# Kernel optimization log

Hardware: AMD Instinct MI355X
Metric: run time of the kernel (lower is better)

Reference implementation:

```python
import jax, jax.numpy as jnp
import numpy as np

N = 50000
E = 800000
IN_CH = 128
HID = 64
HEADS = 4
NEG_SLOPE_GAT = 0.2   # PyG GATConv default negative_slope
NEG_SLOPE_ACT = 0.01  # nn.LeakyReLU default
LN_EPS = 1e-5


def segment_softmax(logits, seg, num):
    # softmax over edges grouped by destination node (PyG softmax semantics)
    m = jax.ops.segment_max(logits, seg, num_segments=num)
    m = jnp.where(jnp.isfinite(m), m, 0.0)
    e = jnp.exp(logits - m[seg])
    s = jax.ops.segment_sum(e, seg, num_segments=num)
    return e / (s[seg] + 1e-16)


def gat_conv(x, edge_index, W, a_src, a_dst, b, heads, out_ch):
    n = x.shape[0]
    loop = jnp.arange(n)
    src = jnp.concatenate([edge_index[0], loop])  # message sources (x_j)
    dst = jnp.concatenate([edge_index[1], loop])  # aggregation targets (x_i)
    h = (x @ W).reshape(n, heads, out_ch)          # [N,H,C]
    alpha_src = (h * a_src).sum(-1)                # [N,H]
    alpha_dst = (h * a_dst).sum(-1)                # [N,H]
    alpha = alpha_src[src] + alpha_dst[dst]        # [E',H]
    alpha = jax.nn.leaky_relu(alpha, NEG_SLOPE_GAT)
    alpha = segment_softmax(alpha, dst, n)
    msg = h[src] * alpha[:, :, None]               # [E',H,C] gathered messages
    out = jax.ops.segment_sum(msg, dst, num_segments=n)  # [N,H,C]
    return out.reshape(n, heads * out_ch) + b


def layer_norm(x, gamma, beta):
    mu = x.mean(-1, keepdims=True)
    var = ((x - mu) ** 2).mean(-1, keepdims=True)
    return (x - mu) * jax.lax.rsqrt(var + LN_EPS) * gamma + beta


def setup_inputs() -> dict:
    key = jax.random.key(0)
    ks = jax.random.split(key, 12)
    d1 = HEADS * HID
    inp = {
        "x": jax.random.normal(ks[0], (N, IN_CH), dtype=jnp.float32),
        "edge_index": jax.random.randint(ks[1], (2, E), 0, N, dtype=jnp.int64),
        "W1": jax.random.normal(ks[2], (IN_CH, d1), dtype=jnp.float32) * 0.05,
        "a_src1": jax.random.normal(ks[3], (HEADS, HID), dtype=jnp.float32) * 0.1,
        "a_dst1": jax.random.normal(ks[4], (HEADS, HID), dtype=jnp.float32) * 0.1,
        "b1": jnp.zeros((d1,), dtype=jnp.float32),
        "gamma": jnp.ones((d1,), dtype=jnp.float32),
        "beta": jnp.zeros((d1,), dtype=jnp.float32),
        "W2": jax.random.normal(ks[5], (d1, HID), dtype=jnp.float32) * 0.05,
        "a_src2": jax.random.normal(ks[6], (1, HID), dtype=jnp.float32) * 0.1,
        "a_dst2": jax.random.normal(ks[7], (1, HID), dtype=jnp.float32) * 0.1,
        "b2": jnp.zeros((HID,), dtype=jnp.float32),
    }
    return inp


def reference(x, edge_index, W1, a_src1, a_dst1, b1, gamma, beta, W2, a_src2, a_dst2, b2):
    h = gat_conv(x, edge_index, W1, a_src1, a_dst1, b1, HEADS, HID)  # [N, H*HID]
    h = layer_norm(h, gamma, beta)
    h = jax.nn.leaky_relu(h, NEG_SLOPE_ACT)
    out = gat_conv(h, edge_index, W2, a_src2, a_dst2, b2, 1, HID)    # [N, HID]
    return out
```

## Files before the change

kernel.cpp:

```cpp
#include <hip/hip_runtime.h>
#include <hip/hip_bf16.h>

#define IN_CH 128
#define D1 256
#define HID 64
#define HEADS 4

typedef _Float16 h16;
typedef __attribute__((ext_vector_type(4))) _Float16 half4v;
typedef __attribute__((ext_vector_type(8))) _Float16 half8v;
typedef __attribute__((ext_vector_type(4))) float f32x4;

__device__ __forceinline__ float lrelu02(float v) { return v > 0.f ? v : 0.2f * v; }
__device__ __forceinline__ float lrelu001(float v) { return v > 0.f ? v : 0.01f * v; }

__global__ __launch_bounds__(256) void setup_kernel(const float* __restrict__ W1,
                                                    const float* __restrict__ W2,
                                                    const float* __restrict__ a_src1,
                                                    const float* __restrict__ a_dst1,
                                                    const float* __restrict__ a_src2,
                                                    const float* __restrict__ a_dst2,
                                                    const int* __restrict__ ei,
                                                    int* __restrict__ cnt,
                                                    h16* __restrict__ w1t,
                                                    h16* __restrict__ w2t,
                                                    int nE) {
    const int b = blockIdx.x;
    const int t = threadIdx.x;
    if (b == 0) {
        for (int k = 0; k < IN_CH; ++k) w1t[t * IN_CH + k] = (h16)W1[k * D1 + t];
    } else if (b == 1) {
        if (t < HID)
            for (int k = 0; k < D1; ++k) w2t[t * D1 + k] = (h16)W2[k * HID + t];
        for (int i = t; i < 14 * D1; i += 256) w2t[66 * D1 + i] = (h16)0.f;
    } else if (b == 2) {
        for (int o = t; o < 1024; o += 256) {
            int v = o >> 7, k = o & 127;
            int h = v & 3;
            const float* avec = (v >> 2) ? (a_dst1 + h * HID) : (a_src1 + h * HID);
            const float* wrow = W1 + k * D1 + h * HID;
            float s = 0.f;
            for (int c = 0; c < HID; ++c) s += wrow[c] * avec[c];
            w1t[(256 + v) * IN_CH + k] = (h16)s;
            w1t[(264 + v) * IN_CH + k] = (h16)0.f;
        }
    } else if (b == 3) {
        for (int o = t; o < 512; o += 256) {
            int v = o >> 8, k = o & 255;
            const float* avec = v ? a_dst2 : a_src2;
            const float* wrow = W2 + k * HID;
            float s = 0.f;
            for (int c = 0; c < HID; ++c) s += wrow[c] * avec[c];
            w2t[(64 + v) * D1 + k] = (h16)s;
        }
    } else {
        int e = (b - 4) * 256 + t;
        if (e < nE) atomicAdd(&cnt[ei[nE + e]], 1);
    }
}

__global__ __launch_bounds__(256) void assign_gemm1_kernel(
        int* __restrict__ cursor,
        int* __restrict__ rowStart, int* __restrict__ rowEnd,
        int* __restrict__ srcIdx, int* __restrict__ gcount,
        float* __restrict__ asad2, int n, int nbAssign,
        const float* __restrict__ x, const h16* __restrict__ w1t,
        h16* __restrict__ h1, float* __restrict__ asad) {
    if (blockIdx.x < (unsigned)nbAssign) {
        const int t = threadIdx.x;
        const int lane = t & 63;
        const int base = blockIdx.x * 1024 + t * 4;
        int d[4], dp[4];
        int tsum = 0;
        #pragma unroll
        for (int q = 0; q < 4; ++q) {
            int i = base + q;
            d[q] = (i < n) ? cursor[i] : 0;
            dp[q] = (d[q] + 3) & ~3;
            tsum += dp[q];
        }
        int incl = tsum;
        #pragma unroll
        for (int off = 1; off < 64; off <<= 1) {
            int y = __shfl_up(incl, off, 64);
            if (lane >= off) incl += y;
        }
        int total = __shfl(incl, 63, 64);
        int wbase = 0;
        if (lane == 63) wbase = atomicAdd(gcount, total);
        wbase = __shfl(wbase, 63, 64);
        int start = wbase + (incl - tsum);
        #pragma unroll
        for (int q = 0; q < 4; ++q) {
            int i = base + q;
            if (i < n) {
                rowStart[i] = start;
                cursor[i] = start;
                rowEnd[i] = start + dp[q];
                for (int p = d[q]; p < dp[q]; ++p) srcIdx[start + p] = n;
                start += dp[q];
            }
        }
        if (blockIdx.x == 0 && t == 0) {
            asad2[(size_t)n * 2] = -1e30f;
            asad2[(size_t)n * 2 + 1] = -1e30f;
        }
        return;
    }
    const int bid = blockIdx.x - nbAssign;
    const int wave = threadIdx.x >> 6, lane = threadIdx.x & 63;
    const int r = lane & 15, ksel = lane >> 4;
    const int rowBase = bid * 64 + wave * 16;
    const int row_a = rowBase + r;
    half8v a[4];
    if (row_a < n) {
        const float* xrow = x + (size_t)row_a * IN_CH + ksel * 8;
        #pragma unroll
        for (int kk = 0; kk < 4; ++kk) {
            float4 u = *(const float4*)(xrow + kk * 32);
            float4 v = *(const float4*)(xrow + kk * 32 + 4);
            half8v av;
            av[0] = (h16)u.x; av[1] = (h16)u.y; av[2] = (h16)u.z; av[3] = (h16)u.w;
            av[4] = (h16)v.x; av[5] = (h16)v.y; av[6] = (h16)v.z; av[7] = (h16)v.w;
            a[kk] = av;
        }
    } else {
        #pragma unroll
        for (int kk = 0; kk < 4; ++kk) a[kk] = (half8v){};
    }
    f32x4 acc[17];
    #pragma unroll
    for (int ct = 0; ct < 17; ++ct) acc[ct] = (f32x4){0.f, 0.f, 0.f, 0.f};
    #pragma unroll
    for (int ct = 0; ct < 17; ++ct) {
        const h16* wrow = w1t + (size_t)(ct * 16 + r) * IN_CH + ksel * 8;
        #pragma unroll
        for (int kk = 0; kk < 4; ++kk) {
            half8v b = *(const half8v*)(wrow + kk * 32);
            acc[ct] = __builtin_amdgcn_mfma_f32_16x16x32_f16(a[kk], b, acc[ct], 0, 0, 0);
        }
    }
    #pragma unroll
    for (int i = 0; i < 4; ++i) {
        int row = rowBase + ksel * 4 + i;
        if (row < n) {
            #pragma unroll
            for (int ct = 0; ct < 16; ++ct)
                h1[(size_t)row * D1 + ct * 16 + r] = (h16)acc[ct][i];
            if (r < 8) asad[(size_t)row * 8 + r] = acc[16][i];
        }
    }
}

__global__ __launch_bounds__(256) void scatter_ewt_kernel(const int* __restrict__ ei,
                                                          int* __restrict__ cursor,
                                                          const float* __restrict__ asad,
                                                          int* __restrict__ srcIdx,
                                                          h16* __restrict__ wE1, int nE) {
    int e = blockIdx.x * 256 + threadIdx.x;
    if (e >= nE) return;
    int src = ei[e];
    int dst = ei[nE + e];
    int pos = atomicAdd(&cursor[dst], 1);
    srcIdx[pos] = src;
    float4 as = *(const float4*)&asad[(size_t)src * 8];
    float4 ad = *(const float4*)&asad[(size_t)dst * 8 + 4];
    half4v w;
    w.x = (h16)expf(lrelu02(as.x + ad.x));
    w.y = (h16)expf(lrelu02(as.y + ad.y));
    w.z = (h16)expf(lrelu02(as.z + ad.z));
    w.w = (h16)expf(lrelu02(as.w + ad.w));
    *(half4v*)&wE1[(size_t)pos * 4] = w;
}

__global__ __launch_bounds__(256) void gemm2_mfma(const h16* __restrict__ hm,
                                                  const h16* __restrict__ w2t,
                                                  h16* __restrict__ h2,
                                                  float* __restrict__ asad2, int n) {
    const int wave = threadIdx.x >> 6, lane = threadIdx.x & 63;
    const int r = lane & 15, ksel = lane >> 4;
    const int rowBase = blockIdx.x * 64 + wave * 16;
    const h16* xrow = hm + (size_t)(rowBase + r) * D1 + ksel * 8;
    half8v a[8];
    #pragma unroll
    for (int kk = 0; kk < 8; ++kk) a[kk] = *(const half8v*)(xrow + kk * 32);
    f32x4 acc[5];
    #pragma unroll
    for (int ct = 0; ct < 5; ++ct) acc[ct] = (f32x4){0.f, 0.f, 0.f, 0.f};
    #pragma unroll
    for (int ct = 0; ct < 5; ++ct) {
        const h16* wrow = w2t + (size_t)(ct * 16 + r) * D1 + ksel * 8;
        #pragma unroll
        for (int kk = 0; kk < 8; ++kk) {
            half8v b = *(const half8v*)(wrow + kk * 32);
            acc[ct] = __builtin_amdgcn_mfma_f32_16x16x32_f16(a[kk], b, acc[ct], 0, 0, 0);
        }
    }
    #pragma unroll
    for (int i = 0; i < 4; ++i) {
        int row = rowBase + ksel * 4 + i;
        if (row < n) {
            #pragma unroll
            for (int ct = 0; ct < 4; ++ct)
                h2[(size_t)row * HID + ct * 16 + r] = (h16)acc[ct][i];
            if (r < 2) asad2[(size_t)row * 2 + r] = acc[4][i];
        }
    }
}

__global__ __launch_bounds__(256) void gather1_kernel(const h16* __restrict__ h1,
                                                      const float* __restrict__ asad,
                                                      const h16* __restrict__ wE1,
                                                      const int* __restrict__ rowStart,
                                                      const int* __restrict__ rowEnd,
                                                      const int* __restrict__ srcIdx,
                                                      const float* __restrict__ b1,
                                                      const float* __restrict__ gamma,
                                                      const float* __restrict__ beta,
                                                      h16* __restrict__ hmid,
                                                      int n, int npad) {
    const int lane = threadIdx.x & 63;
    const int node = (blockIdx.x * 256 + threadIdx.x) >> 6;
    if (node >= npad) return;
    if (node >= n) {
        half4v z = {};
        *(half4v*)&hmid[(size_t)node * D1 + lane * 4] = z;
        return;
    }
    const int hh = lane >> 4;
    const float wself = expf(lrelu02(asad[(size_t)node * 8 + hh] +
                                     asad[(size_t)node * 8 + 4 + hh]));
    half4v sv = *(const half4v*)&h1[(size_t)node * D1 + lane * 4];
    h16 wsh = (h16)wself;
    half4v acc = sv * (half4v){wsh, wsh, wsh, wsh};
    float den = wself;
    const int beg = rowStart[node], end = rowEnd[node];
    int j = beg;
    for (; j + 8 <= end; j += 8) {
        int4 ia = *(const int4*)&srcIdx[j];
        int4 ib = *(const int4*)&srcIdx[j + 4];
        h16 w0 = wE1[(size_t)(j + 0) * 4 + hh];
        h16 w1 = wE1[(size_t)(j + 1) * 4 + hh];
        h16 w2 = wE1[(size_t)(j + 2) * 4 + hh];
        h16 w3 = wE1[(size_t)(j + 3) * 4 + hh];
        h16 w4 = wE1[(size_t)(j + 4) * 4 + hh];
        h16 w5 = wE1[(size_t)(j + 5) * 4 + hh];
        h16 w6 = wE1[(size_t)(j + 6) * 4 + hh];
        h16 w7 = wE1[(size_t)(j + 7) * 4 + hh];
        half4v r0 = *(const half4v*)&h1[(size_t)ia.x * D1 + lane * 4];
        half4v r1 = *(const half4v*)&h1[(size_t)ia.y * D1 + lane * 4];
        half4v r2 = *(const half4v*)&h1[(size_t)ia.z * D1 + lane * 4];
        half4v r3 = *(const half4v*)&h1[(size_t)ia.w * D1 + lane * 4];
        half4v r4 = *(const half4v*)&h1[(size_t)ib.x * D1 + lane * 4];
        half4v r5 = *(const half4v*)&h1[(size_t)ib.y * D1 + lane * 4];
        half4v r6 = *(const half4v*)&h1[(size_t)ib.z * D1 + lane * 4];
        half4v r7 = *(const half4v*)&h1[(size_t)ib.w * D1 + lane * 4];
        acc += r0 * (half4v){w0, w0, w0, w0};
        acc += r1 * (half4v){w1, w1, w1, w1};
        acc += r2 * (half4v){w2, w2, w2, w2};
        acc += r3 * (half4v){w3, w3, w3, w3};
        acc += r4 * (half4v){w4, w4, w4, w4};
        acc += r5 * (half4v){w5, w5, w5, w5};
        acc += r6 * (half4v){w6, w6, w6, w6};
        acc += r7 * (half4v){w7, w7, w7, w7};
        den += (float)w0 + (float)w1 + (float)w2 + (float)w3
             + (float)w4 + (float)w5 + (float)w6 + (float)w7;
    }
    if (j < end) {
        int4 ia = *(const int4*)&srcIdx[j];
        h16 w0 = wE1[(size_t)(j + 0) * 4 + hh];
        h16 w1 = wE1[(size_t)(j + 1) * 4 + hh];
        h16 w2 = wE1[(size_t)(j + 2) * 4 + hh];
        h16 w3 = wE1[(size_t)(j + 3) * 4 + hh];
        half4v r0 = *(const half4v*)&h1[(size_t)ia.x * D1 + lane * 4];
        half4v r1 = *(const half4v*)&h1[(size_t)ia.y * D1 + lane * 4];
        half4v r2 = *(const half4v*)&h1[(size_t)ia.z * D1 + lane * 4];
        half4v r3 = *(const half4v*)&h1[(size_t)ia.w * D1 + lane * 4];
        acc += r0 * (half4v){w0, w0, w0, w0};
        acc += r1 * (half4v){w1, w1, w1, w1};
        acc += r2 * (half4v){w2, w2, w2, w2};
        acc += r3 * (half4v){w3, w3, w3, w3};
        den += (float)w0 + (float)w1 + (float)w2 + (float)w3;
    }
    float4 accf = make_float4((float)acc[0], (float)acc[1], (float)acc[2], (float)acc[3]);
    float inv = 1.f / (den + 1e-16f);
    float4 bv = *(const float4*)&b1[lane * 4];
    float4 y;
    y.x = accf.x * inv + bv.x; y.y = accf.y * inv + bv.y;
    y.z = accf.z * inv + bv.z; y.w = accf.w * inv + bv.w;
    float s = y.x + y.y + y.z + y.w;
    #pragma unroll
    for (int off = 1; off < 64; off <<= 1) s += __shfl_xor(s, off, 64);
    float mu = s * (1.f / 256.f);
    float4 dx;
    dx.x = y.x - mu; dx.y = y.y - mu; dx.z = y.z - mu; dx.w = y.w - mu;
    float sq = dx.x * dx.x + dx.y * dx.y + dx.z * dx.z + dx.w * dx.w;
    #pragma unroll
    for (int off = 1; off < 64; off <<= 1) sq += __shfl_xor(sq, off, 64);
    float rs = rsqrtf(sq * (1.f / 256.f) + 1e-5f);
    float4 g = *(const float4*)&gamma[lane * 4];
    float4 be = *(const float4*)&beta[lane * 4];
    half4v o;
    o.x = (h16)lrelu001(dx.x * rs * g.x + be.x);
    o.y = (h16)lrelu001(dx.y * rs * g.y + be.y);
    o.z = (h16)lrelu001(dx.z * rs * g.z + be.z);
    o.w = (h16)lrelu001(dx.w * rs * g.w + be.w);
    *(half4v*)&hmid[(size_t)node * D1 + lane * 4] = o;
}

__global__ __launch_bounds__(256) void gather2_kernel(const h16* __restrict__ h2,
                                                      const float* __restrict__ asad2,
                                                      const int* __restrict__ rowStart,
                                                      const int* __restrict__ rowEnd,
                                                      const int* __restrict__ srcIdx,
                                                      const float* __restrict__ b2,
                                                      float* __restrict__ out, int n) {
    const int lane = threadIdx.x & 63;
    const int node = (blockIdx.x * 256 + threadIdx.x) >> 6;
    if (node >= n) return;
    const int li = lane & 15, eh = lane >> 4;
    const int c0 = li * 4;
    const float ad_n = asad2[(size_t)node * 2 + 1];
    float acc[4] = {0.f, 0.f, 0.f, 0.f};
    float den = 0.f;
    if (eh == 0) {
        float w0 = expf(lrelu02(asad2[(size_t)node * 2] + ad_n));
        half4v sv = *(const half4v*)&h2[(size_t)node * HID + c0];
        #pragma unroll
        for (int i = 0; i < 4; ++i) acc[i] = (float)sv[i] * w0;
        den = w0;
    }
    const int beg = rowStart[node], end = rowEnd[node];
    int j = beg;
    for (; j + 8 <= end; j += 8) {
        int e0 = j + eh, e1 = j + 4 + eh;
        int s0 = srcIdx[e0], s1 = srcIdx[e1];
        float a0 = asad2[(size_t)s0 * 2], a1 = asad2[(size_t)s1 * 2];
        half4v r0 = *(const half4v*)&h2[(size_t)s0 * HID + c0];
        half4v r1 = *(const half4v*)&h2[(size_t)s1 * HID + c0];
        float w0 = expf(lrelu02(a0 + ad_n));
        float w1 = expf(lrelu02(a1 + ad_n));
        #pragma unroll
        for (int i = 0; i < 4; ++i) {
            acc[i] = fmaf((float)r0[i], w0, acc[i]);
            acc[i] = fmaf((float)r1[i], w1, acc[i]);
        }
        den += w0 + w1;
    }
    if (j < end) {
        int e = j + eh;
        int s = srcIdx[e];
        float w = expf(lrelu02(asad2[(size_t)s * 2] + ad_n));
        half4v r = *(const half4v*)&h2[(size_t)s * HID + c0];
        #pragma unroll
        for (int i = 0; i < 4; ++i) acc[i] = fmaf((float)r[i], w, acc[i]);
        den += w;
    }
    #pragma unroll
    for (int i = 0; i < 4; ++i) {
        acc[i] += __shfl_xor(acc[i], 32, 64);
        acc[i] += __shfl_xor(acc[i], 16, 64);
    }
    den += __shfl_xor(den, 32, 64);
    den += __shfl_xor(den, 16, 64);
    if (lane < 16) {
        float inv = 1.f / (den + 1e-16f);
        float4 bv = *(const float4*)&b2[c0];
        float4 o;
        o.x = acc[0] * inv + bv.x;
        o.y = acc[1] * inv + bv.y;
        o.z = acc[2] * inv + bv.z;
        o.w = acc[3] * inv + bv.w;
        *(float4*)&out[(size_t)node * HID + c0] = o;
    }
}

extern "C" void kernel_launch(void* const* d_in, const int* in_sizes, int n_in,
                              void* d_out, int out_size, void* d_ws, size_t ws_size,
                              hipStream_t stream) {
    const float* x      = (const float*)d_in[0];
    const int*   ei     = (const int*)d_in[1];
    const float* W1     = (const float*)d_in[2];
    const float* a_src1 = (const float*)d_in[3];
    const float* a_dst1 = (const float*)d_in[4];
    const float* b1     = (const float*)d_in[5];
    const float* gamma  = (const float*)d_in[6];
    const float* beta   = (const float*)d_in[7];
    const float* W2     = (const float*)d_in[8];
    const float* a_src2 = (const float*)d_in[9];
    const float* a_dst2 = (const float*)d_in[10];
    const float* b2     = (const float*)d_in[11];
    float* out = (float*)d_out;

    const int N = in_sizes[0] / IN_CH;
    const int E = in_sizes[1] / 2;
    const int NP = (N + 63) & ~63;
    const int Emax = E + 3 * N + 16;

    float* ws = (float*)d_ws;
    size_t off = 0;
    h16*   h1   = (h16*)(ws + off); off += (size_t)128 * (N + 1);
    h16*   hmid = (h16*)(ws + off); off += (size_t)128 * NP;
    h16*   h2   = (h16*)(ws + off); off += (size_t)32 * (N + 1);
    float* asad = ws + off;         off += (size_t)8 * N;
    float* asad2= ws + off;         off += (size_t)2 * (N + 1);
    int* rowStart  = (int*)(ws + off); off += N;
    int* rowEnd    = (int*)(ws + off); off += N;
    h16* w1t = (h16*)(ws + off); off += 17408;
    h16* w2t = (h16*)(ws + off); off += 10240;
    int* gcount = (int*)(ws + off); off += 1;
    int* cursor = (int*)(ws + off); off += N;
    int* srcIdx = (int*)(ws + off); off += Emax;
    h16* wE1    = (h16*)(ws + off); off += (size_t)2 * Emax;
    const size_t memsetBytes = ((size_t)1 + N + Emax) * 4 + (size_t)4 * Emax * 2;

    const int nodeBlocks  = (N + 3) / 4;
    const int nodeBlocksP = (NP + 3) / 4;
    const int nThreadBlocksE = (E + 255) / 256;
    const int nbAssign = (N + 1023) / 1024;

    hipMemsetAsync(gcount, 0, memsetBytes, stream);
    setup_kernel<<<4 + nThreadBlocksE, 256, 0, stream>>>(
        W1, W2, a_src1, a_dst1, a_src2, a_dst2, ei, cursor, w1t, w2t, E);
    assign_gemm1_kernel<<<nbAssign + NP / 64, 256, 0, stream>>>(
        cursor, rowStart, rowEnd, srcIdx, gcount, asad2, N, nbAssign,
        x, w1t, h1, asad);
    scatter_ewt_kernel<<<nThreadBlocksE, 256, 0, stream>>>(ei, cursor, asad, srcIdx,
                                                           wE1, E);
    gather1_kernel<<<nodeBlocksP, 256, 0, stream>>>(h1, asad, wE1, rowStart, rowEnd,
                                                    srcIdx, b1, gamma, beta, hmid, N, NP);
    gemm2_mfma<<<NP / 64, 256, 0, stream>>>(hmid, w2t, h2, asad2, N);
    gather2_kernel<<<nodeBlocks, 256, 0, stream>>>(h2, asad2, rowStart, rowEnd, srcIdx,
                                                   b2, out, N);
}
```

Measured before the change: 258.3 us.

## Overlap edge scatter with GEMM1 and compute edge weights in a separate pass

Moves the CSR assignment into its own kernel and fuses the edge scatter, which now also records each slot's destination, with the first GEMM. This lets scatter overlap with the matmul, since scatter no longer needs the attention logits. Edge weights are then computed over all slots in a new kernel that zeroes padding and out-of-range slots, so the large memset of the srcIdx and wE1 buffers can be dropped. In exchange it adds an extra launch plus a dstIdx write and read, and the weight kernel runs over every allocated slot, including unused ones.

```diff
diff --git a/kernel.cpp b/kernel.cpp
--- a/kernel.cpp
+++ b/kernel.cpp
@@ -59,55 +59,68 @@
     }
 }
 
-__global__ __launch_bounds__(256) void assign_gemm1_kernel(
-        int* __restrict__ cursor,
-        int* __restrict__ rowStart, int* __restrict__ rowEnd,
-        int* __restrict__ srcIdx, int* __restrict__ gcount,
-        float* __restrict__ asad2, int n, int nbAssign,
+__global__ __launch_bounds__(256) void assign_kernel(int* __restrict__ cursor,
+                                                     int* __restrict__ rowStart,
+                                                     int* __restrict__ rowEnd,
+                                                     int* __restrict__ srcIdx,
+                                                     int* __restrict__ gcount,
+                                                     float* __restrict__ asad2, int n) {
+    const int t = threadIdx.x;
+    const int lane = t & 63;
+    const int base = blockIdx.x * 1024 + t * 4;
+    int d[4], dp[4];
+    int tsum = 0;
+    #pragma unroll
+    for (int q = 0; q < 4; ++q) {
+        int i = base + q;
+        d[q] = (i < n) ? cursor[i] : 0;
+        dp[q] = (d[q] + 3) & ~3;
+        tsum += dp[q];
+    }
+    int incl = tsum;
+    #pragma unroll
+    for (int off = 1; off < 64; off <<= 1) {
+        int y = __shfl_up(incl, off, 64);
+        if (lane >= off) incl += y;
+    }
+    int total = __shfl(incl, 63, 64);
+    int wbase = 0;
+    if (lane == 63) wbase = atomicAdd(gcount, total);
+    wbase = __shfl(wbase, 63, 64);
+    int start = wbase + (incl - tsum);
+    #pragma unroll
+    for (int q = 0; q < 4; ++q) {
+        int i = base + q;
+        if (i < n) {
+            rowStart[i] = start;
+            cursor[i] = start;
+            rowEnd[i] = start + dp[q];
+            for (int p = d[q]; p < dp[q]; ++p) srcIdx[start + p] = n;
+            start += dp[q];
+        }
+    }
+    if (blockIdx.x == 0 && t == 0) {
+        asad2[(size_t)n * 2] = -1e30f;
+        asad2[(size_t)n * 2 + 1] = -1e30f;
+    }
+}
+
+__global__ __launch_bounds__(256) void scatter_gemm1_kernel(
+        const int* __restrict__ ei, int* __restrict__ cursor,
+        int* __restrict__ srcIdx, int* __restrict__ dstIdx, int nE, int nbScatter,
         const float* __restrict__ x, const h16* __restrict__ w1t,
-        h16* __restrict__ h1, float* __restrict__ asad) {
-    if (blockIdx.x < (unsigned)nbAssign) {
-        const int t = threadIdx.x;
-        const int lane = t & 63;
-        const int base = blockIdx.x * 1024 + t * 4;
-        int d[4], dp[4];
-        int tsum = 0;
-        #pragma unroll
-        for (int q = 0; q < 4; ++q) {
-            int i = base + q;
-            d[q] = (i < n) ? cursor[i] : 0;
-            dp[q] = (d[q] + 3) & ~3;
-            tsum += dp[q];
-        }
-        int incl = tsum;
-        #pragma unroll
-        for (int off = 1; off < 64; off <<= 1) {
-            int y = __shfl_up(incl, off, 64);
-            if (lane >= off) incl += y;
-        }
-        int total = __shfl(incl, 63, 64);
-        int wbase = 0;
-        if (lane == 63) wbase = atomicAdd(gcount, total);
-        wbase = __shfl(wbase, 63, 64);
-        int start = wbase + (incl - tsum);
-        #pragma unroll
-        for (int q = 0; q < 4; ++q) {
-            int i = base + q;
-            if (i < n) {
-                rowStart[i] = start;
-                cursor[i] = start;
-                rowEnd[i] = start + dp[q];
-                for (int p = d[q]; p < dp[q]; ++p) srcIdx[start + p] = n;
-                start += dp[q];
-            }
-        }
-        if (blockIdx.x == 0 && t == 0) {
-            asad2[(size_t)n * 2] = -1e30f;
-            asad2[(size_t)n * 2 + 1] = -1e30f;
-        }
+        h16* __restrict__ h1, float* __restrict__ asad, int n) {
+    if (blockIdx.x < (unsigned)nbScatter) {
+        int e = blockIdx.x * 256 + threadIdx.x;
+        if (e >= nE) return;
+        int src = ei[e];
+        int dst = ei[nE + e];
+        int pos = atomicAdd(&cursor[dst], 1);
+        srcIdx[pos] = src;
+        dstIdx[pos] = dst;
         return;
     }
-    const int bid = blockIdx.x - nbAssign;
+    const int bid = blockIdx.x - nbScatter;
     const int wave = threadIdx.x >> 6, lane = threadIdx.x & 63;
     const int r = lane & 15, ksel = lane >> 4;
     const int rowBase = bid * 64 + wave * 16;
@@ -152,25 +165,27 @@
     }
 }
 
-__global__ __launch_bounds__(256) void scatter_ewt_kernel(const int* __restrict__ ei,
-                                                          int* __restrict__ cursor,
-                                                          const float* __restrict__ asad,
-                                                          int* __restrict__ srcIdx,
-                                                          h16* __restrict__ wE1, int nE) {
+__global__ __launch_bounds__(256) void ewt1_kernel(const int* __restrict__ srcIdx,
+                                                   const int* __restrict__ dstIdx,
+                                                   const float* __restrict__ asad,
+                                                   h16* __restrict__ wE1,
+                                                   int nSlots, int n) {
     int e = blockIdx.x * 256 + threadIdx.x;
-    if (e >= nE) return;
-    int src = ei[e];
-    int dst = ei[nE + e];
-    int pos = atomicAdd(&cursor[dst], 1);
-    srcIdx[pos] = src;
-    float4 as = *(const float4*)&asad[(size_t)src * 8];
-    float4 ad = *(const float4*)&asad[(size_t)dst * 8 + 4];
+    if (e >= nSlots) return;
+    int s = srcIdx[e];
+    int d = dstIdx[e];
+    if ((unsigned)s >= (unsigned)n || (unsigned)d >= (unsigned)n) {
+        *(half4v*)&wE1[(size_t)e * 4] = (half4v){};
+        return;
+    }
+    float4 as = *(const float4*)&asad[(size_t)s * 8];
+    float4 ad = *(const float4*)&asad[(size_t)d * 8 + 4];
     half4v w;
     w.x = (h16)expf(lrelu02(as.x + ad.x));
     w.y = (h16)expf(lrelu02(as.y + ad.y));
     w.z = (h16)expf(lrelu02(as.z + ad.z));
     w.w = (h16)expf(lrelu02(as.w + ad.w));
-    *(half4v*)&wE1[(size_t)pos * 4] = w;
+    *(half4v*)&wE1[(size_t)e * 4] = w;
 }
 
 __global__ __launch_bounds__(256) void gemm2_mfma(const h16* __restrict__ hm,
@@ -408,11 +423,12 @@
     int* rowEnd    = (int*)(ws + off); off += N;
     h16* w1t = (h16*)(ws + off); off += 17408;
     h16* w2t = (h16*)(ws + off); off += 10240;
+    int* srcIdx = (int*)(ws + off); off += Emax;
+    int* dstIdx = (int*)(ws + off); off += Emax;
+    h16* wE1    = (h16*)(ws + off); off += (size_t)2 * Emax;
     int* gcount = (int*)(ws + off); off += 1;
     int* cursor = (int*)(ws + off); off += N;
-    int* srcIdx = (int*)(ws + off); off += Emax;
-    h16* wE1    = (h16*)(ws + off); off += (size_t)2 * Emax;
-    const size_t memsetBytes = ((size_t)1 + N + Emax) * 4 + (size_t)4 * Emax * 2;
+    const size_t memsetBytes = ((size_t)1 + N) * 4;
 
     const int nodeBlocks  = (N + 3) / 4;
     const int nodeBlocksP = (NP + 3) / 4;
@@ -422,11 +438,12 @@
     hipMemsetAsync(gcount, 0, memsetBytes, stream);
     setup_kernel<<<4 + nThreadBlocksE, 256, 0, stream>>>(
         W1, W2, a_src1, a_dst1, a_src2, a_dst2, ei, cursor, w1t, w2t, E);
-    assign_gemm1_kernel<<<nbAssign + NP / 64, 256, 0, stream>>>(
-        cursor, rowStart, rowEnd, srcIdx, gcount, asad2, N, nbAssign,
-        x, w1t, h1, asad);
-    scatter_ewt_kernel<<<nThreadBlocksE, 256, 0, stream>>>(ei, cursor, asad, srcIdx,
-                                                           wE1, E);
+    assign_kernel<<<nbAssign, 256, 0, stream>>>(cursor, rowStart, rowEnd, srcIdx,
+                                                gcount, asad2, N);
+    scatter_gemm1_kernel<<<nThreadBlocksE + NP / 64, 256, 0, stream>>>(
+        ei, cursor, srcIdx, dstIdx, E, nThreadBlocksE, x, w1t, h1, asad, N);
+    ewt1_kernel<<<(Emax + 255) / 256, 256, 0, stream>>>(srcIdx, dstIdx, asad,
+                                                        wE1, Emax, N);
     gather1_kernel<<<nodeBlocksP, 256, 0, stream>>>(h1, asad, wE1, rowStart, rowEnd,
                                                     srcIdx, b1, gamma, beta, hmid, N, NP);
     gemm2_mfma<<<NP / 64, 256, 0, stream>>>(hmid, w2t, h2, asad2, N);
```

After: 276.9 us. 7.2% more time.
